# Kernel tuning notes

Hardware: AMD Instinct MI355X
Metric: run time of the kernel (lower is better)

## Reference

```python
import jax, jax.numpy as jnp
import numpy as np

DIM = 1024
NUM_HEADS = 16
HEAD_DIM = DIM // NUM_HEADS
ROPE_BASE = 10000.0


def _rope_cos_sin(seq_len, head_dim, dtype):
    # inv_freq over even indices of head_dim
    inv_freq = 1.0 / (ROPE_BASE ** (jnp.arange(0, head_dim, 2, dtype=jnp.float32) / head_dim))
    t = jnp.arange(seq_len, dtype=jnp.float32)
    freqs = jnp.einsum('i,j->ij', t, inv_freq)        # [N, D/2]
    emb = jnp.concatenate([freqs, freqs], axis=-1)    # [N, D]
    return jnp.cos(emb).astype(dtype), jnp.sin(emb).astype(dtype)


def _rotate_half(x):
    x1, x2 = jnp.split(x, 2, axis=-1)
    return jnp.concatenate([-x2, x1], axis=-1)


def setup_inputs() -> dict:
    key = jax.random.key(0)
    k1, k2, k3 = jax.random.split(key, 3)
    B, N = 2, 2048
    x = jax.random.normal(k1, (B, N, DIM), dtype=jnp.float32)
    # torch Linear weights: [out_features, in_features]; init scale ~1/sqrt(dim)
    Wqkv = jax.random.normal(k2, (3 * DIM, DIM), dtype=jnp.float32) * (DIM ** -0.5)
    Wproj = jax.random.normal(k3, (DIM, DIM), dtype=jnp.float32) * (DIM ** -0.5)
    return {"x": x, "Wqkv": Wqkv, "Wproj": Wproj}


def reference(x, Wqkv, Wproj):
    B, N, C = x.shape
    H, D = NUM_HEADS, HEAD_DIM
    # QKV projection: [B,N,3C] -> [3,B,H,N,D]
    qkv = jnp.einsum('bnc,oc->bno', x, Wqkv)
    qkv = qkv.reshape(B, N, 3, H, D).transpose(2, 0, 3, 1, 4)
    q, k, v = qkv[0], qkv[1], qkv[2]                  # each [B,H,N,D]
    # RoPE
    cos, sin = _rope_cos_sin(N, D, x.dtype)           # [N,D] each
    cos = cos[None, None, :, :]
    sin = sin[None, None, :, :]
    q = q * cos + _rotate_half(q) * sin
    k = k * cos + _rotate_half(k) * sin
    # scaled dot-product attention (non-causal, no mask, no dropout)
    scale = 1.0 / jnp.sqrt(jnp.asarray(D, dtype=x.dtype))
    scores = jnp.einsum('bhnd,bhmd->bhnm', q, k) * scale
    attn = jax.nn.softmax(scores, axis=-1)
    out = jnp.einsum('bhnm,bhmd->bhnd', attn, v)      # [B,H,N,D]
    out = out.transpose(0, 2, 1, 3).reshape(B, N, C)
    return jnp.einsum('bnc,oc->bno', out, Wproj)
```

## Files before the change

### kernel.cpp

```cpp
#include <hip/hip_runtime.h>
#include <hip/hip_bf16.h>

#define SEQ   2048
#define DIMC  1024
#define NH    16
#define HD    64
#define QKV3  3072
#define NB    2
#define SCALE_LOG2E 0.18033688011112042f

typedef __attribute__((ext_vector_type(8)))  short bf16x8;
typedef __attribute__((ext_vector_type(4)))  float f32x4;
typedef __attribute__((ext_vector_type(16))) float f32x16;

__device__ __forceinline__ unsigned short f2bf(float f){
  union { float f; unsigned int u; } v; v.f = f;
  return (unsigned short)((v.u + 0x7fffu + ((v.u >> 16) & 1u)) >> 16);
}
__device__ __forceinline__ float bf2f(unsigned short h){
  union { unsigned int u; float f; } v; v.u = ((unsigned int)h) << 16; return v.f;
}
__device__ __forceinline__ int packbf2(float a, float b){
  __hip_bfloat162 h = __float22bfloat162_rn(make_float2(a, b));
  int r; __builtin_memcpy(&r, &h, 4); return r;
}
__device__ __forceinline__ void async_lds16(void* lds, const void* g){
  __builtin_amdgcn_global_load_lds(
      (const __attribute__((address_space(1))) void*)g,
      (__attribute__((address_space(3))) void*)lds, 16, 0, 0);
}

__global__ __launch_bounds__(256) void k_cvt(const float* __restrict__ in,
                                             unsigned short* __restrict__ out, int n4){
  int i = blockIdx.x * 256 + threadIdx.x;
  if (i >= n4) return;
  const float4 v = ((const float4*)in)[i];
  union { unsigned short s[4]; unsigned long long u; } p;
  p.s[0] = f2bf(v.x); p.s[1] = f2bf(v.y); p.s[2] = f2bf(v.z); p.s[3] = f2bf(v.w);
  *(unsigned long long*)(out + (size_t)i * 4) = p.u;
}

__global__ __launch_bounds__(256) void k_tab(float2* __restrict__ tab){
  int idx = blockIdx.x * 256 + threadIdx.x;
  int n = idx >> 5, j = idx & 31;
  float inv = 1.0f / powf(10000.0f, (float)(2 * j) * (1.0f / 64.0f));
  float f = (float)n * inv;
  tab[idx] = make_float2(cosf(f), sinf(f));
}

template<int OUT_BF16>
__global__ __launch_bounds__(256) void k_gemm(const unsigned short* __restrict__ A,
                                              const unsigned short* __restrict__ Bm,
                                              void* __restrict__ Cp, int M, int N, int K){
  __shared__ unsigned short As[128 * 64];
  __shared__ unsigned short Bs[128 * 64];
  const int tid = threadIdx.x, wave = tid >> 6, lane = tid & 63;
  const int nbn = N >> 7;
  const int bm = blockIdx.x / nbn, bn = blockIdx.x % nbn;
  const int m0 = bm << 7, n0 = bn << 7;
  const int wr = wave >> 1, wc = wave & 1;

  f32x4 acc[4][4];
#pragma unroll
  for (int i = 0; i < 4; i++)
#pragma unroll
    for (int j = 0; j < 4; j++) acc[i][j] = (f32x4){0.f, 0.f, 0.f, 0.f};

  for (int k0 = 0; k0 < K; k0 += 64){
#pragma unroll
    for (int c = 0; c < 4; c++){
      const int e = c * 2048 + tid * 8;
      const int row = e >> 6, col = e & 63;
      async_lds16(As + c * 2048 + wave * 512, A + (size_t)(m0 + row) * K + k0 + col);
      async_lds16(Bs + c * 2048 + wave * 512, Bm + (size_t)(n0 + row) * K + k0 + col);
    }
    __syncthreads();
#pragma unroll
    for (int ks = 0; ks < 2; ks++){
      const int kk = ks * 32 + (lane >> 4) * 8;
      bf16x8 af[4], bfr[4];
#pragma unroll
      for (int i = 0; i < 4; i++){
        af[i]  = *(const bf16x8*)&As[(wr * 64 + i * 16 + (lane & 15)) * 64 + kk];
        bfr[i] = *(const bf16x8*)&Bs[(wc * 64 + i * 16 + (lane & 15)) * 64 + kk];
      }
#pragma unroll
      for (int i = 0; i < 4; i++)
#pragma unroll
        for (int j = 0; j < 4; j++)
          acc[i][j] = __builtin_amdgcn_mfma_f32_16x16x32_bf16(af[i], bfr[j], acc[i][j], 0, 0, 0);
    }
    __syncthreads();
  }
#pragma unroll
  for (int i = 0; i < 4; i++)
#pragma unroll
    for (int j = 0; j < 4; j++)
#pragma unroll
      for (int r = 0; r < 4; r++){
        const int row = m0 + wr * 64 + i * 16 + (lane >> 4) * 4 + r;
        const int col = n0 + wc * 64 + j * 16 + (lane & 15);
        const float v = acc[i][j][r];
        if constexpr (OUT_BF16) ((unsigned short*)Cp)[(size_t)row * N + col] = f2bf(v);
        else                    ((float*)Cp)[(size_t)row * N + col] = v;
      }
}

__global__ __launch_bounds__(256) void k_rope(const unsigned short* __restrict__ qkv,
                                              const float2* __restrict__ tab,
                                              unsigned short* __restrict__ Qb,
                                              unsigned short* __restrict__ Kswz){
  unsigned int idx = blockIdx.x * 256 + threadIdx.x;
  const int j = idx & 3; idx >>= 2;
  const int n = idx & 2047; idx >>= 11;
  const int h = idx & 15; idx >>= 4;
  const int b = idx & 1;
  const int which = idx >> 1;
  const size_t rowbase = ((size_t)(b * SEQ + n)) * QKV3 + which * DIMC + h * HD;
  const bf16x8 lo = *(const bf16x8*)&qkv[rowbase + j * 8];
  const bf16x8 hi = *(const bf16x8*)&qkv[rowbase + 32 + j * 8];
  union { unsigned short s[8]; bf16x8 v; } olo, ohi;
#pragma unroll
  for (int t = 0; t < 8; t++){
    const float2 cs = tab[n * 32 + j * 8 + t];
    const float xl = bf2f((unsigned short)lo[t]), xh = bf2f((unsigned short)hi[t]);
    float yl = xl * cs.x - xh * cs.y;
    float yh = xh * cs.x + xl * cs.y;
    if (which == 0){ yl *= SCALE_LOG2E; yh *= SCALE_LOG2E; }
    olo.s[t] = f2bf(yl); ohi.s[t] = f2bf(yh);
  }
  const size_t orow = (((size_t)(b * NH + h)) * SEQ + n) * HD;
  if (which == 0){
    *(bf16x8*)&Qb[orow + j * 8]      = olo.v;
    *(bf16x8*)&Qb[orow + 32 + j * 8] = ohi.v;
  } else {
    const int s = (n & 7) << 3;
    *(bf16x8*)&Kswz[orow + ((j * 8) ^ s)]      = olo.v;
    *(bf16x8*)&Kswz[orow + ((32 + j * 8) ^ s)] = ohi.v;
  }
}

__global__ __launch_bounds__(256) void k_vt(const unsigned short* __restrict__ qkv,
                                            unsigned short* __restrict__ Vt){
  __shared__ unsigned short t[64 * 72];
  const int tid = threadIdx.x;
  const int nt = blockIdx.x & 31, h = (blockIdx.x >> 5) & 15, b = blockIdx.x >> 9;
  const int n0 = nt * 64;
#pragma unroll
  for (int p = 0; p < 2; p++){
    const int e = p * 2048 + tid * 8;
    const int r = e >> 6, c = e & 63;
    *(bf16x8*)&t[r * 72 + c] =
        *(const bf16x8*)&qkv[((size_t)(b * SEQ + n0 + r)) * QKV3 + 2048 + h * 64 + c];
  }
  __syncthreads();
#pragma unroll
  for (int p = 0; p < 2; p++){
    const int e = p * 2048 + tid * 8;
    const int d = e >> 6, nn = e & 63;
    const int sw = (d & 7) << 3;
    union { unsigned short s[8]; bf16x8 v; } o;
#pragma unroll
    for (int q = 0; q < 8; q++) o.s[q] = t[((nn ^ sw) + q) * 72 + d];
    *(bf16x8*)&Vt[(((size_t)(b * NH + h)) * HD + d) * SEQ + n0 + nn] = o.v;
  }
}

__global__ __launch_bounds__(256) void k_attn(const unsigned short* __restrict__ Q,
                                              const unsigned short* __restrict__ Kg,
                                              const unsigned short* __restrict__ Vg,
                                              unsigned short* __restrict__ AO){
  __shared__ unsigned short Ks[64 * 64];
  __shared__ unsigned short Vs[64 * 64];
  const int tid = threadIdx.x, wave = tid >> 6, lane = tid & 63;
  const int bh = blockIdx.x & 31, qt = blockIdx.x >> 5;
  const size_t base = (size_t)bh * (SEQ * HD);
  const int q32 = lane & 31, hi = lane >> 5, hi8 = hi << 3;
  const int sw = (q32 & 7) << 3;
  const int q0w = qt * 128 + wave * 32;

  bf16x8 qf[4];
#pragma unroll
  for (int kc = 0; kc < 4; kc++)
    qf[kc] = *(const bf16x8*)&Q[base + (size_t)(q0w + q32) * HD + kc * 16 + hi8];

  f32x16 oacc[2];
#pragma unroll
  for (int md = 0; md < 2; md++)
#pragma unroll
    for (int r = 0; r < 16; r++) oacc[md][r] = 0.f;
  float mrow = -INFINITY, lrow = 0.f;

  const int srow = lane >> 3, scol = (lane & 7) * 8;

  for (int kv0 = 0; kv0 < SEQ; kv0 += 64){
#pragma unroll
    for (int i = 0; i < 2; i++){
      const int c = wave * 2 + i;
      const int row = c * 8 + srow;
      async_lds16(&Ks[c * 512], &Kg[base + (size_t)(kv0 + row) * HD + scol]);
      async_lds16(&Vs[c * 512], &Vg[base + (size_t)row * SEQ + kv0 + scol]);
    }
    __syncthreads();

    f32x16 s0, s1;
#pragma unroll
    for (int r = 0; r < 16; r++){ s0[r] = 0.f; s1[r] = 0.f; }
#pragma unroll
    for (int kc = 0; kc < 4; kc++){
      const int col = (kc * 16 + hi8) ^ sw;
      const bf16x8 k0 = *(const bf16x8*)&Ks[q32 * 64 + col];
      const bf16x8 k1 = *(const bf16x8*)&Ks[(32 + q32) * 64 + col];
      s0 = __builtin_amdgcn_mfma_f32_32x32x16_bf16(k0, qf[kc], s0, 0, 0, 0);
      s1 = __builtin_amdgcn_mfma_f32_32x32x16_bf16(k1, qf[kc], s1, 0, 0, 0);
    }

    float mx = fmaxf(s0[0], s0[1]);
#pragma unroll
    for (int r = 2; r < 16; r++) mx = fmaxf(mx, s0[r]);
#pragma unroll
    for (int r = 0; r < 16; r++) mx = fmaxf(mx, s1[r]);
    mx = fmaxf(mx, __shfl_xor(mx, 32));
    const float mnew = fmaxf(mrow, mx);
    const float alpha = __builtin_amdgcn_exp2f(mrow - mnew);
#pragma unroll
    for (int r = 0; r < 16; r++){
      s0[r] = __builtin_amdgcn_exp2f(s0[r] - mnew);
      s1[r] = __builtin_amdgcn_exp2f(s1[r] - mnew);
    }
    float rs = 0.f;
#pragma unroll
    for (int r = 0; r < 16; r++) rs += s0[r] + s1[r];
    rs += __shfl_xor(rs, 32);
    lrow = lrow * alpha + rs;
    mrow = mnew;
#pragma unroll
    for (int md = 0; md < 2; md++)
#pragma unroll
      for (int r = 0; r < 16; r++) oacc[md][r] *= alpha;

#pragma unroll
    for (int g2 = 0; g2 < 4; g2++){
      float pj[8];
#pragma unroll
      for (int t = 0; t < 8; t++) pj[t] = (g2 < 2) ? s0[(g2 & 1) * 8 + t] : s1[(g2 & 1) * 8 + t];
      const int X0 = packbf2(pj[0], pj[1]), X1 = packbf2(pj[2], pj[3]);
      const int Y0 = packbf2(pj[4], pj[5]), Y1 = packbf2(pj[6], pj[7]);
      const int pX0 = __shfl_xor(X0, 32), pX1 = __shfl_xor(X1, 32);
      const int pY0 = __shfl_xor(Y0, 32), pY1 = __shfl_xor(Y1, 32);
      union { int w[4]; bf16x8 v; } pb;
      pb.w[0] = hi ? pY0 : X0;
      pb.w[1] = hi ? pY1 : X1;
      pb.w[2] = hi ? Y0 : pX0;
      pb.w[3] = hi ? Y1 : pX1;
#pragma unroll
      for (int md = 0; md < 2; md++){
        const bf16x8 av = *(const bf16x8*)&Vs[(md * 32 + q32) * 64 + ((g2 * 16 + hi8) ^ sw)];
        oacc[md] = __builtin_amdgcn_mfma_f32_32x32x16_bf16(av, pb.v, oacc[md], 0, 0, 0);
      }
    }
    __syncthreads();
  }

  const float rl = 1.0f / lrow;
  const int b = bh >> 4, h = bh & 15;
  const size_t obase = ((size_t)(b * SEQ + q0w + q32)) * DIMC + h * HD;
#pragma unroll
  for (int md = 0; md < 2; md++)
#pragma unroll
    for (int a = 0; a < 4; a++){
      const int d0 = md * 32 + a * 8 + hi * 4;
      int2 wv;
      wv.x = packbf2(oacc[md][a * 4 + 0] * rl, oacc[md][a * 4 + 1] * rl);
      wv.y = packbf2(oacc[md][a * 4 + 2] * rl, oacc[md][a * 4 + 3] * rl);
      *(int2*)&AO[obase + d0] = wv;
    }
}

extern "C" void kernel_launch(void* const* d_in, const int* in_sizes, int n_in,
                              void* d_out, int out_size, void* d_ws, size_t ws_size,
                              hipStream_t stream){
  const float* x     = (const float*)d_in[0];
  const float* Wqkv  = (const float*)d_in[1];
  const float* Wproj = (const float*)d_in[2];
  float* out = (float*)d_out;
  char* ws = (char*)d_ws;

  unsigned short* xb     = (unsigned short*)(ws);
  unsigned short* wqkvb  = (unsigned short*)(ws +  8388608);
  unsigned short* wprojb = (unsigned short*)(ws + 14680064);
  unsigned short* qkvb   = (unsigned short*)(ws + 16777216);
  float2*         tab    = (float2*)        (ws + 41943040);
  unsigned short* Qb     = (unsigned short*)(ws + 42467328);
  unsigned short* Kb     = (unsigned short*)(ws + 50855936);
  unsigned short* Vtb    = (unsigned short*)(ws + 59244544);
  unsigned short* AOb    = (unsigned short*)(ws);

  k_cvt<<<4096, 256, 0, stream>>>(x, xb, 1048576);
  k_cvt<<<3072, 256, 0, stream>>>(Wqkv, wqkvb, 786432);
  k_cvt<<<1024, 256, 0, stream>>>(Wproj, wprojb, 262144);
  k_tab<<<256, 256, 0, stream>>>(tab);
  k_gemm<1><<<32 * 24, 256, 0, stream>>>(xb, wqkvb, (void*)qkvb, 4096, 3072, 1024);
  k_rope<<<2048, 256, 0, stream>>>(qkvb, tab, Qb, Kb);
  k_vt<<<1024, 256, 0, stream>>>(qkvb, Vtb);
  k_attn<<<512, 256, 0, stream>>>(Qb, Kb, Vtb, AOb);
  k_gemm<0><<<32 * 8, 256, 0, stream>>>(AOb, wprojb, (void*)out, 4096, 1024, 1024);
}
```

Measured before the change: 237.3 us.

## Load K/V fragments straight to registers with double-buffering, dropping LDS staging

The attention kernel no longer stages K and V tiles through shared memory with barriers. Each wave loads its MFMA fragments directly from global memory into registers, with K double-buffered one tile ahead. V is pre-tiled by k_vt into 64x64 blocks so these loads are contiguous, and the K/V swizzles are removed. The change also adds s_setprio around MFMAs, skips the rescale when the running max is unchanged, uses tree reductions, and sets launch_bounds(256,2). The cost is more register pressure, and every wave now reads the same K/V data from L2 separately instead of sharing it through LDS.

Result: slower. 288.6 us (+21.6%).

```diff
diff --git a/kernel.cpp b/kernel.cpp
--- a/kernel.cpp
+++ b/kernel.cpp
@@ -109,7 +109,7 @@
 __global__ __launch_bounds__(256) void k_rope(const unsigned short* __restrict__ qkv,
                                               const float2* __restrict__ tab,
                                               unsigned short* __restrict__ Qb,
-                                              unsigned short* __restrict__ Kswz){
+                                              unsigned short* __restrict__ Kb){
   unsigned int idx = blockIdx.x * 256 + threadIdx.x;
   const int j = idx & 3; idx >>= 2;
   const int n = idx & 2047; idx >>= 11;
@@ -130,14 +130,9 @@
     olo.s[t] = f2bf(yl); ohi.s[t] = f2bf(yh);
   }
   const size_t orow = (((size_t)(b * NH + h)) * SEQ + n) * HD;
-  if (which == 0){
-    *(bf16x8*)&Qb[orow + j * 8]      = olo.v;
-    *(bf16x8*)&Qb[orow + 32 + j * 8] = ohi.v;
-  } else {
-    const int s = (n & 7) << 3;
-    *(bf16x8*)&Kswz[orow + ((j * 8) ^ s)]      = olo.v;
-    *(bf16x8*)&Kswz[orow + ((32 + j * 8) ^ s)] = ohi.v;
-  }
+  unsigned short* dst = which ? Kb : Qb;
+  *(bf16x8*)&dst[orow + j * 8]      = olo.v;
+  *(bf16x8*)&dst[orow + 32 + j * 8] = ohi.v;
 }
 
 __global__ __launch_bounds__(256) void k_vt(const unsigned short* __restrict__ qkv,
@@ -158,31 +153,30 @@
   for (int p = 0; p < 2; p++){
     const int e = p * 2048 + tid * 8;
     const int d = e >> 6, nn = e & 63;
-    const int sw = (d & 7) << 3;
     union { unsigned short s[8]; bf16x8 v; } o;
 #pragma unroll
-    for (int q = 0; q < 8; q++) o.s[q] = t[((nn ^ sw) + q) * 72 + d];
-    *(bf16x8*)&Vt[(((size_t)(b * NH + h)) * HD + d) * SEQ + n0 + nn] = o.v;
-  }
-}
-
-__global__ __launch_bounds__(256) void k_attn(const unsigned short* __restrict__ Q,
-                                              const unsigned short* __restrict__ Kg,
-                                              const unsigned short* __restrict__ Vg,
-                                              unsigned short* __restrict__ AO){
-  __shared__ unsigned short Ks[64 * 64];
-  __shared__ unsigned short Vs[64 * 64];
+    for (int q = 0; q < 8; q++) o.s[q] = t[(nn + q) * 72 + d];
+    *(bf16x8*)&Vt[(((size_t)(b * NH + h) * 32 + nt) * 64 + d) * 64 + nn] = o.v;
+  }
+}
+
+struct KF { bf16x8 f[8]; };
+struct VF { bf16x8 f[8]; };
+
+__global__ __launch_bounds__(256, 2) void k_attn(const unsigned short* __restrict__ Q,
+                                                 const unsigned short* __restrict__ Kg,
+                                                 const unsigned short* __restrict__ Vg,
+                                                 unsigned short* __restrict__ AO){
   const int tid = threadIdx.x, wave = tid >> 6, lane = tid & 63;
   const int bh = blockIdx.x & 31, qt = blockIdx.x >> 5;
-  const size_t base = (size_t)bh * (SEQ * HD);
+  const size_t kbase = (size_t)bh * (SEQ * HD);
   const int q32 = lane & 31, hi = lane >> 5, hi8 = hi << 3;
-  const int sw = (q32 & 7) << 3;
   const int q0w = qt * 128 + wave * 32;
 
   bf16x8 qf[4];
 #pragma unroll
   for (int kc = 0; kc < 4; kc++)
-    qf[kc] = *(const bf16x8*)&Q[base + (size_t)(q0w + q32) * HD + kc * 16 + hi8];
+    qf[kc] = *(const bf16x8*)&Q[kbase + (size_t)(q0w + q32) * HD + kc * 16 + hi8];
 
   f32x16 oacc[2];
 #pragma unroll
@@ -191,54 +185,67 @@
     for (int r = 0; r < 16; r++) oacc[md][r] = 0.f;
   float mrow = -INFINITY, lrow = 0.f;
 
-  const int srow = lane >> 3, scol = (lane & 7) * 8;
-
-  for (int kv0 = 0; kv0 < SEQ; kv0 += 64){
-#pragma unroll
-    for (int i = 0; i < 2; i++){
-      const int c = wave * 2 + i;
-      const int row = c * 8 + srow;
-      async_lds16(&Ks[c * 512], &Kg[base + (size_t)(kv0 + row) * HD + scol]);
-      async_lds16(&Vs[c * 512], &Vg[base + (size_t)row * SEQ + kv0 + scol]);
-    }
-    __syncthreads();
-
+  const unsigned short* kp = Kg + kbase + (size_t)q32 * HD + hi8;
+  const unsigned short* vp = Vg + (size_t)bh * (32 * 4096) + q32 * 64 + hi8;
+
+  KF kA, kB;
+  VF vv;
+
+  auto loadK = [&](KF& d, int kv0){
+#pragma unroll
+    for (int kp2 = 0; kp2 < 2; kp2++)
+#pragma unroll
+      for (int kc = 0; kc < 4; kc++)
+        d.f[kp2 * 4 + kc] = *(const bf16x8*)&kp[(size_t)(kv0 + kp2 * 32) * HD + kc * 16];
+  };
+  auto loadV = [&](VF& d, int t){
+#pragma unroll
+    for (int g2 = 0; g2 < 4; g2++)
+#pragma unroll
+      for (int md = 0; md < 2; md++)
+        d.f[g2 * 2 + md] = *(const bf16x8*)&vp[t * 4096 + md * 2048 + g2 * 16];
+  };
+
+  auto tile = [&](const KF& kf, const VF& vf){
     f32x16 s0, s1;
 #pragma unroll
     for (int r = 0; r < 16; r++){ s0[r] = 0.f; s1[r] = 0.f; }
+    __builtin_amdgcn_s_setprio(1);
 #pragma unroll
     for (int kc = 0; kc < 4; kc++){
-      const int col = (kc * 16 + hi8) ^ sw;
-      const bf16x8 k0 = *(const bf16x8*)&Ks[q32 * 64 + col];
-      const bf16x8 k1 = *(const bf16x8*)&Ks[(32 + q32) * 64 + col];
-      s0 = __builtin_amdgcn_mfma_f32_32x32x16_bf16(k0, qf[kc], s0, 0, 0, 0);
-      s1 = __builtin_amdgcn_mfma_f32_32x32x16_bf16(k1, qf[kc], s1, 0, 0, 0);
-    }
-
-    float mx = fmaxf(s0[0], s0[1]);
-#pragma unroll
-    for (int r = 2; r < 16; r++) mx = fmaxf(mx, s0[r]);
-#pragma unroll
-    for (int r = 0; r < 16; r++) mx = fmaxf(mx, s1[r]);
+      s0 = __builtin_amdgcn_mfma_f32_32x32x16_bf16(kf.f[kc],     qf[kc], s0, 0, 0, 0);
+      s1 = __builtin_amdgcn_mfma_f32_32x32x16_bf16(kf.f[4 + kc], qf[kc], s1, 0, 0, 0);
+    }
+    __builtin_amdgcn_s_setprio(0);
+    float m8[8];
+#pragma unroll
+    for (int r = 0; r < 8; r++)
+      m8[r] = fmaxf(fmaxf(s0[r], s0[r + 8]), fmaxf(s1[r], s1[r + 8]));
+    float mx = fmaxf(fmaxf(fmaxf(m8[0], m8[4]), fmaxf(m8[1], m8[5])),
+                     fmaxf(fmaxf(m8[2], m8[6]), fmaxf(m8[3], m8[7])));
     mx = fmaxf(mx, __shfl_xor(mx, 32));
-    const float mnew = fmaxf(mrow, mx);
-    const float alpha = __builtin_amdgcn_exp2f(mrow - mnew);
+    if (!__all(mx <= mrow)){
+      const float mnew = fmaxf(mrow, mx);
+      const float alpha = __builtin_amdgcn_exp2f(mrow - mnew);
+      mrow = mnew;
+      lrow *= alpha;
+#pragma unroll
+      for (int md = 0; md < 2; md++)
+#pragma unroll
+        for (int r = 0; r < 16; r++) oacc[md][r] *= alpha;
+    }
 #pragma unroll
     for (int r = 0; r < 16; r++){
-      s0[r] = __builtin_amdgcn_exp2f(s0[r] - mnew);
-      s1[r] = __builtin_amdgcn_exp2f(s1[r] - mnew);
-    }
-    float rs = 0.f;
-#pragma unroll
-    for (int r = 0; r < 16; r++) rs += s0[r] + s1[r];
+      s0[r] = __builtin_amdgcn_exp2f(s0[r] - mrow);
+      s1[r] = __builtin_amdgcn_exp2f(s1[r] - mrow);
+    }
+    float a8[8];
+#pragma unroll
+    for (int r = 0; r < 8; r++)
+      a8[r] = (s0[r] + s0[r + 8]) + (s1[r] + s1[r + 8]);
+    float rs = ((a8[0] + a8[1]) + (a8[2] + a8[3])) + ((a8[4] + a8[5]) + (a8[6] + a8[7]));
     rs += __shfl_xor(rs, 32);
-    lrow = lrow * alpha + rs;
-    mrow = mnew;
-#pragma unroll
-    for (int md = 0; md < 2; md++)
-#pragma unroll
-      for (int r = 0; r < 16; r++) oacc[md][r] *= alpha;
-
+    lrow += rs;
 #pragma unroll
     for (int g2 = 0; g2 < 4; g2++){
       float pj[8];
@@ -253,13 +260,30 @@
       pb.w[1] = hi ? pY1 : X1;
       pb.w[2] = hi ? Y0 : pX0;
       pb.w[3] = hi ? Y1 : pX1;
-#pragma unroll
-      for (int md = 0; md < 2; md++){
-        const bf16x8 av = *(const bf16x8*)&Vs[(md * 32 + q32) * 64 + ((g2 * 16 + hi8) ^ sw)];
-        oacc[md] = __builtin_amdgcn_mfma_f32_32x32x16_bf16(av, pb.v, oacc[md], 0, 0, 0);
-      }
-    }
-    __syncthreads();
+      __builtin_amdgcn_s_setprio(1);
+#pragma unroll
+      for (int md = 0; md < 2; md++)
+        oacc[md] = __builtin_amdgcn_mfma_f32_32x32x16_bf16(vf.f[g2 * 2 + md], pb.v, oacc[md], 0, 0, 0);
+      __builtin_amdgcn_s_setprio(0);
+    }
+  };
+
+  loadK(kA, 0);
+#pragma unroll 1
+  for (int t2 = 0; t2 < 16; t2++){
+    {
+      const int t = 2 * t2;
+      loadV(vv, t);
+      loadK(kB, (t + 1) * 64);
+      tile(kA, vv);
+    }
+    {
+      const int t = 2 * t2 + 1;
+      loadV(vv, t);
+      const int tn = (t < 31) ? t + 1 : 31;
+      loadK(kA, tn * 64);
+      tile(kB, vv);
+    }
   }
 
   const float rl = 1.0f / lrow;
```

## Double-buffer attention K/V tiles, skip redundant rescales, and merge prep kernels

Applied to the files above, without the earlier changes.

The attention kernel now keeps two LDS buffers for K and V and prefetches the next 64-key tile while computing on the current one, which removes the load-then-sync stall at each iteration. The online-softmax rescale of the accumulators is skipped when no row maximum grows. Max and sum reductions are rebalanced into trees, and s_setprio is raised around the MFMA blocks. The three convert launches and the RoPE-table launch are merged into one prep kernel to cut launch overhead. The cost is doubled LDS per block and a wave-uniform branch in the loop.

After: 238.5 us. No clear change (+0.5%).

```diff
diff --git a/kernel.cpp b/kernel.cpp
--- a/kernel.cpp
+++ b/kernel.cpp
@@ -30,22 +30,30 @@
       (__attribute__((address_space(3))) void*)lds, 16, 0, 0);
 }
 
-__global__ __launch_bounds__(256) void k_cvt(const float* __restrict__ in,
-                                             unsigned short* __restrict__ out, int n4){
-  int i = blockIdx.x * 256 + threadIdx.x;
-  if (i >= n4) return;
-  const float4 v = ((const float4*)in)[i];
-  union { unsigned short s[4]; unsigned long long u; } p;
-  p.s[0] = f2bf(v.x); p.s[1] = f2bf(v.y); p.s[2] = f2bf(v.z); p.s[3] = f2bf(v.w);
-  *(unsigned long long*)(out + (size_t)i * 4) = p.u;
-}
-
-__global__ __launch_bounds__(256) void k_tab(float2* __restrict__ tab){
-  int idx = blockIdx.x * 256 + threadIdx.x;
-  int n = idx >> 5, j = idx & 31;
-  float inv = 1.0f / powf(10000.0f, (float)(2 * j) * (1.0f / 64.0f));
-  float f = (float)n * inv;
-  tab[idx] = make_float2(cosf(f), sinf(f));
+__global__ __launch_bounds__(256) void k_prep(const float* __restrict__ x,
+                                              const float* __restrict__ wqkv,
+                                              const float* __restrict__ wproj,
+                                              unsigned short* __restrict__ xb,
+                                              unsigned short* __restrict__ wqkvb,
+                                              unsigned short* __restrict__ wprojb,
+                                              float2* __restrict__ tab){
+  const int b = blockIdx.x, tid = threadIdx.x;
+  if (b < 8192){
+    const float* in; unsigned short* out; int i;
+    if (b < 4096)      { in = x;     out = xb;     i = b * 256 + tid; }
+    else if (b < 7168) { in = wqkv;  out = wqkvb;  i = (b - 4096) * 256 + tid; }
+    else               { in = wproj; out = wprojb; i = (b - 7168) * 256 + tid; }
+    const float4 v = ((const float4*)in)[i];
+    union { unsigned short s[4]; unsigned long long u; } p;
+    p.s[0] = f2bf(v.x); p.s[1] = f2bf(v.y); p.s[2] = f2bf(v.z); p.s[3] = f2bf(v.w);
+    *(unsigned long long*)(out + (size_t)i * 4) = p.u;
+  } else {
+    const int idx = (b - 8192) * 256 + tid;
+    const int n = idx >> 5, j = idx & 31;
+    const float inv = 1.0f / powf(10000.0f, (float)(2 * j) * (1.0f / 64.0f));
+    const float f = (float)n * inv;
+    tab[idx] = make_float2(cosf(f), sinf(f));
+  }
 }
 
 template<int OUT_BF16>
@@ -170,8 +178,8 @@
                                               const unsigned short* __restrict__ Kg,
                                               const unsigned short* __restrict__ Vg,
                                               unsigned short* __restrict__ AO){
-  __shared__ unsigned short Ks[64 * 64];
-  __shared__ unsigned short Vs[64 * 64];
+  __shared__ unsigned short Ks[2][64 * 64];
+  __shared__ unsigned short Vs[2][64 * 64];
   const int tid = threadIdx.x, wave = tid >> 6, lane = tid & 63;
   const int bh = blockIdx.x & 31, qt = blockIdx.x >> 5;
   const size_t base = (size_t)bh * (SEQ * HD);
@@ -193,57 +201,77 @@
 
   const int srow = lane >> 3, scol = (lane & 7) * 8;
 
-  for (int kv0 = 0; kv0 < SEQ; kv0 += 64){
-#pragma unroll
-    for (int i = 0; i < 2; i++){
-      const int c = wave * 2 + i;
-      const int row = c * 8 + srow;
-      async_lds16(&Ks[c * 512], &Kg[base + (size_t)(kv0 + row) * HD + scol]);
-      async_lds16(&Vs[c * 512], &Vg[base + (size_t)row * SEQ + kv0 + scol]);
-    }
-    __syncthreads();
+#pragma unroll
+  for (int i = 0; i < 2; i++){
+    const int c = wave * 2 + i, row = c * 8 + srow;
+    async_lds16(&Ks[0][c * 512], &Kg[base + (size_t)row * HD + scol]);
+    async_lds16(&Vs[0][c * 512], &Vg[base + (size_t)row * SEQ + scol]);
+  }
+  asm volatile("s_waitcnt vmcnt(0)" ::: "memory");
+  __syncthreads();
+
+#pragma unroll 1
+  for (int t = 0; t < 32; t++){
+    const int cur = t & 1;
+    if (t < 31){
+      const int kv0 = (t + 1) * 64;
+#pragma unroll
+      for (int i = 0; i < 2; i++){
+        const int c = wave * 2 + i, row = c * 8 + srow;
+        async_lds16(&Ks[cur ^ 1][c * 512], &Kg[base + (size_t)(kv0 + row) * HD + scol]);
+        async_lds16(&Vs[cur ^ 1][c * 512], &Vg[base + (size_t)row * SEQ + kv0 + scol]);
+      }
+    }
 
     f32x16 s0, s1;
 #pragma unroll
     for (int r = 0; r < 16; r++){ s0[r] = 0.f; s1[r] = 0.f; }
+    __builtin_amdgcn_s_setprio(1);
 #pragma unroll
     for (int kc = 0; kc < 4; kc++){
       const int col = (kc * 16 + hi8) ^ sw;
-      const bf16x8 k0 = *(const bf16x8*)&Ks[q32 * 64 + col];
-      const bf16x8 k1 = *(const bf16x8*)&Ks[(32 + q32) * 64 + col];
+      const bf16x8 k0 = *(const bf16x8*)&Ks[cur][q32 * 64 + col];
+      const bf16x8 k1 = *(const bf16x8*)&Ks[cur][(32 + q32) * 64 + col];
       s0 = __builtin_amdgcn_mfma_f32_32x32x16_bf16(k0, qf[kc], s0, 0, 0, 0);
       s1 = __builtin_amdgcn_mfma_f32_32x32x16_bf16(k1, qf[kc], s1, 0, 0, 0);
     }
-
-    float mx = fmaxf(s0[0], s0[1]);
-#pragma unroll
-    for (int r = 2; r < 16; r++) mx = fmaxf(mx, s0[r]);
-#pragma unroll
-    for (int r = 0; r < 16; r++) mx = fmaxf(mx, s1[r]);
+    __builtin_amdgcn_s_setprio(0);
+
+    float m8[8];
+#pragma unroll
+    for (int r = 0; r < 8; r++)
+      m8[r] = fmaxf(fmaxf(s0[r], s0[r + 8]), fmaxf(s1[r], s1[r + 8]));
+    float mx = fmaxf(fmaxf(fmaxf(m8[0], m8[4]), fmaxf(m8[1], m8[5])),
+                     fmaxf(fmaxf(m8[2], m8[6]), fmaxf(m8[3], m8[7])));
     mx = fmaxf(mx, __shfl_xor(mx, 32));
-    const float mnew = fmaxf(mrow, mx);
-    const float alpha = __builtin_amdgcn_exp2f(mrow - mnew);
+    if (!__all(mx <= mrow)){
+      const float mnew = fmaxf(mrow, mx);
+      const float alpha = __builtin_amdgcn_exp2f(mrow - mnew);
+      mrow = mnew;
+      lrow *= alpha;
+#pragma unroll
+      for (int md = 0; md < 2; md++)
+#pragma unroll
+        for (int r = 0; r < 16; r++) oacc[md][r] *= alpha;
+    }
 #pragma unroll
     for (int r = 0; r < 16; r++){
-      s0[r] = __builtin_amdgcn_exp2f(s0[r] - mnew);
-      s1[r] = __builtin_amdgcn_exp2f(s1[r] - mnew);
-    }
-    float rs = 0.f;
-#pragma unroll
-    for (int r = 0; r < 16; r++) rs += s0[r] + s1[r];
+      s0[r] = __builtin_amdgcn_exp2f(s0[r] - mrow);
+      s1[r] = __builtin_amdgcn_exp2f(s1[r] - mrow);
+    }
+    float a8[8];
+#pragma unroll
+    for (int r = 0; r < 8; r++)
+      a8[r] = (s0[r] + s0[r + 8]) + (s1[r] + s1[r + 8]);
+    float rs = ((a8[0] + a8[1]) + (a8[2] + a8[3])) + ((a8[4] + a8[5]) + (a8[6] + a8[7]));
     rs += __shfl_xor(rs, 32);
-    lrow = lrow * alpha + rs;
-    mrow = mnew;
-#pragma unroll
-    for (int md = 0; md < 2; md++)
-#pragma unroll
-      for (int r = 0; r < 16; r++) oacc[md][r] *= alpha;
+    lrow += rs;
 
 #pragma unroll
     for (int g2 = 0; g2 < 4; g2++){
       float pj[8];
 #pragma unroll
-      for (int t = 0; t < 8; t++) pj[t] = (g2 < 2) ? s0[(g2 & 1) * 8 + t] : s1[(g2 & 1) * 8 + t];
+      for (int t2 = 0; t2 < 8; t2++) pj[t2] = (g2 < 2) ? s0[(g2 & 1) * 8 + t2] : s1[(g2 & 1) * 8 + t2];
       const int X0 = packbf2(pj[0], pj[1]), X1 = packbf2(pj[2], pj[3]);
       const int Y0 = packbf2(pj[4], pj[5]), Y1 = packbf2(pj[6], pj[7]);
       const int pX0 = __shfl_xor(X0, 32), pX1 = __shfl_xor(X1, 32);
@@ -253,12 +281,16 @@
       pb.w[1] = hi ? pY1 : X1;
       pb.w[2] = hi ? Y0 : pX0;
       pb.w[3] = hi ? Y1 : pX1;
+      __builtin_amdgcn_s_setprio(1);
 #pragma unroll
       for (int md = 0; md < 2; md++){
-        const bf16x8 av = *(const bf16x8*)&Vs[(md * 32 + q32) * 64 + ((g2 * 16 + hi8) ^ sw)];
+        const bf16x8 av = *(const bf16x8*)&Vs[cur][(md * 32 + q32) * 64 + ((g2 * 16 + hi8) ^ sw)];
         oacc[md] = __builtin_amdgcn_mfma_f32_32x32x16_bf16(av, pb.v, oacc[md], 0, 0, 0);
       }
-    }
+      __builtin_amdgcn_s_setprio(0);
+    }
+
+    asm volatile("s_waitcnt vmcnt(0)" ::: "memory");
     __syncthreads();
   }
 
@@ -296,10 +328,7 @@
   unsigned short* Vtb    = (unsigned short*)(ws + 59244544);
   unsigned short* AOb    = (unsigned short*)(ws);
 
-  k_cvt<<<4096, 256, 0, stream>>>(x, xb, 1048576);
-  k_cvt<<<3072, 256, 0, stream>>>(Wqkv, wqkvb, 786432);
-  k_cvt<<<1024, 256, 0, stream>>>(Wproj, wprojb, 262144);
-  k_tab<<<256, 256, 0, stream>>>(tab);
+  k_prep<<<8448, 256, 0, stream>>>(x, Wqkv, Wproj, xb, wqkvb, wprojb, tab);
   k_gemm<1><<<32 * 24, 256, 0, stream>>>(xb, wqkvb, (void*)qkvb, 4096, 3072, 1024);
   k_rope<<<2048, 256, 0, stream>>>(qkvb, tab, Qb, Kb);
   k_vt<<<1024, 256, 0, stream>>>(qkvb, Vtb);
```
